# Kernel tuning notes

Measured on AMD Instinct MI355X. Metric: run time of the kernel, lower is better.

## Reference

```python
import jax, jax.numpy as jnp
import numpy as np

HIDDEN = 4096
N_HEADS = 16
HEAD_DIM = HIDDEN // N_HEADS  # 256
ROTARY_DIM = 64
ROPE_THETA = 10000.0


def _rope_cos_sin(positions):
    # positions: [S] int -> cos/sin: [S, ROTARY_DIM//2]
    inv_freq = 1.0 / (ROPE_THETA ** (jnp.arange(0, ROTARY_DIM, 2, dtype=jnp.float32) / ROTARY_DIM))
    angles = positions.astype(jnp.float32)[:, None] * inv_freq[None, :]
    return jnp.cos(angles), jnp.sin(angles)


def _apply_rope_interleaved(x, cos, sin):
    # x: [B, S, H, D]; rotate first ROTARY_DIM dims, GPT-J (non-neox) interleaved pairs
    xr = x[..., :ROTARY_DIM]
    x1 = xr[..., 0::2]
    x2 = xr[..., 1::2]
    c = cos[None, :, None, :]
    s = sin[None, :, None, :]
    o1 = x1 * c - x2 * s
    o2 = x1 * s + x2 * c
    rot = jnp.stack([o1, o2], axis=-1).reshape(xr.shape)
    return jnp.concatenate([rot, x[..., ROTARY_DIM:]], axis=-1)


def setup_inputs() -> dict:
    key = jax.random.key(0)
    k1, k2, k3 = jax.random.split(key, 3)
    B, S = 2, 2048
    hidden_states = jax.random.normal(k1, (B, S, HIDDEN), dtype=jnp.float32)
    positions = jnp.arange(S, dtype=jnp.int32)
    w_qkv = jax.random.normal(k2, (3 * HIDDEN, HIDDEN), dtype=jnp.float32) * 0.02
    w_out = jax.random.normal(k3, (HIDDEN, HIDDEN), dtype=jnp.float32) * 0.02
    return {"hidden_states": hidden_states, "positions": positions, "w_qkv": w_qkv, "w_out": w_out}


def reference(hidden_states, positions, w_qkv, w_out):
    B, S, H = hidden_states.shape
    qkv = jnp.einsum("bsh,oh->bso", hidden_states, w_qkv)  # [B,S,3H]
    q, k, v = jnp.split(qkv, 3, axis=-1)
    q = q.reshape(B, S, N_HEADS, HEAD_DIM)
    k = k.reshape(B, S, N_HEADS, HEAD_DIM)
    v = v.reshape(B, S, N_HEADS, HEAD_DIM)
    cos, sin = _rope_cos_sin(positions)
    q = _apply_rope_interleaved(q, cos, sin)
    k = _apply_rope_interleaved(k, cos, sin)
    scale = HEAD_DIM ** -0.5
    scores = jnp.einsum("bqhd,bkhd->bhqk", q, k) * scale  # [B,nh,S,S]
    causal = jnp.tril(jnp.ones((S, S), dtype=bool))
    scores = jnp.where(causal[None, None], scores, jnp.finfo(scores.dtype).min)
    probs = jax.nn.softmax(scores, axis=-1)
    attn = jnp.einsum("bhqk,bkhd->bqhd", probs, v).reshape(B, S, H)
    return jnp.einsum("bsh,oh->bso", attn, w_out)
```

## Files before the change

kernel.cpp:

```cpp
#include <hip/hip_runtime.h>

typedef __attribute__((ext_vector_type(8))) short short8;
typedef __attribute__((ext_vector_type(4))) float f32x4;

__device__ __forceinline__ unsigned short f2bf(float f) {
    union { float f; unsigned int u; } v; v.f = f;
    unsigned int u = v.u;
    unsigned int r = (u + 0x7FFFu + ((u >> 16) & 1u)) >> 16;
    return (unsigned short)r;
}
__device__ __forceinline__ float bf2f(unsigned short u) {
    union { unsigned int u; float f; } v; v.u = ((unsigned int)u) << 16;
    return v.f;
}
__device__ __forceinline__ void load_lds16(const void* g, void* l) {
    __builtin_amdgcn_global_load_lds(
        (const __attribute__((address_space(1))) void*)g,
        (__attribute__((address_space(3))) void*)l, 16, 0, 0);
}
#define FENCE() asm volatile("" ::: "memory")
#define BAR() do { FENCE(); __builtin_amdgcn_s_barrier(); FENCE(); } while (0)

__device__ __forceinline__ int swz(int o) { return o ^ ((o >> 3) & 0x70); }

__global__ __launch_bounds__(256) void conv_bf16(const float* __restrict__ in,
                                                 unsigned short* __restrict__ out, int n4) {
    int i = blockIdx.x * 256 + threadIdx.x;
    if (i >= n4) return;
    float4 v = ((const float4*)in)[i];
    ushort4 o;
    o.x = f2bf(v.x); o.y = f2bf(v.y); o.z = f2bf(v.z); o.w = f2bf(v.w);
    ((ushort4*)out)[i] = o;
}

template <bool OUT_BF16>
__global__ __launch_bounds__(512, 2) void gemm256(const unsigned short* __restrict__ A,
                                                  const unsigned short* __restrict__ B,
                                                  void* __restrict__ Cv,
                                                  int M, int N, int K, int NBN) {
    __shared__ __align__(16) char smem[131072];
    const int tid = threadIdx.x;
    const int lane = tid & 63, wv = tid >> 6;
    const int wm = wv >> 2, wn = wv & 3;
    const int fr = lane & 15, fo = (lane >> 4) * 8;

    const int nwg = gridDim.x, bid = blockIdx.x;
    const int q = nwg >> 3, r = nwg & 7, xcd = bid & 7, lid = bid >> 3;
    const int wg = (xcd < r ? xcd * (q + 1) : r * (q + 1) + (xcd - r) * q) + lid;
    const int bm = wg / NBN, bn = wg % NBN;

    const unsigned short* gA = A + (size_t)bm * 256 * K;
    const unsigned short* gB = B + (size_t)bn * 256 * K;

    int srow[2][2], scol[2][2];
#pragma unroll
    for (int h = 0; h < 2; ++h)
#pragma unroll
        for (int rr = 0; rr < 2; ++rr) {
            int o = h * 16384 + rr * 8192 + tid * 16;
            int osw = swz(o);
            srow[h][rr] = osw >> 7;
            scol[h][rr] = (osw & 127) >> 1;
        }

    f32x4 acc[8][4] = {};
    short8 a[4][2], b[4][2];

    auto STAGE = [&](const unsigned short* g, int regionBase, int h, int t) {
#pragma unroll
        for (int rr = 0; rr < 2; ++rr)
            load_lds16(g + (size_t)srow[h][rr] * K + t * 64 + scol[h][rr],
                       smem + regionBase + h * 16384 + rr * 8192 + tid * 16);
    };
    auto RDA = [&](int bufBase, int mh) {
#pragma unroll
        for (int mf = 0; mf < 4; ++mf)
#pragma unroll
            for (int ks = 0; ks < 2; ++ks) {
                int o = swz((wm * 128 + mh * 64 + mf * 16 + fr) * 128 + (ks * 32 + fo) * 2);
                a[mf][ks] = *(const short8*)(smem + bufBase + o);
            }
    };
    auto RDB = [&](int bufBase, int nh) {
#pragma unroll
        for (int jj = 0; jj < 2; ++jj)
#pragma unroll
            for (int ks = 0; ks < 2; ++ks) {
                int o = swz((wn * 64 + (nh * 2 + jj) * 16 + fr) * 128 + (ks * 32 + fo) * 2);
                b[nh * 2 + jj][ks] = *(const short8*)(smem + bufBase + 32768 + o);
            }
    };
    auto MM = [&](int mh, int nh) {
        __builtin_amdgcn_s_setprio(1);
#pragma unroll
        for (int mf = 0; mf < 4; ++mf)
#pragma unroll
            for (int jj = 0; jj < 2; ++jj)
#pragma unroll
                for (int ks = 0; ks < 2; ++ks)
                    acc[mh * 4 + mf][nh * 2 + jj] = __builtin_amdgcn_mfma_f32_16x16x32_bf16(
                        a[mf][ks], b[nh * 2 + jj][ks], acc[mh * 4 + mf][nh * 2 + jj], 0, 0, 0);
        __builtin_amdgcn_s_setprio(0);
    };

    const int A0 = 0, B0 = 32768, A1 = 65536, B1 = 98304;

    STAGE(gA, A0, 0, 0); STAGE(gA, A0, 1, 0);
    STAGE(gB, B0, 0, 0); STAGE(gB, B0, 1, 0);
    STAGE(gB, B1, 0, 1); STAGE(gB, B1, 1, 1);
    FENCE();
    asm volatile("s_waitcnt vmcnt(4)" ::: "memory");
    __builtin_amdgcn_s_barrier();
    FENCE();

    const int NIT = K >> 7;
    for (int i = 0; i < NIT; ++i) {
        const bool last = (i == NIT - 1);
        const int t0 = 2 * i, t1 = 2 * i + 1;
        RDA(A0, 0); RDB(A0, 0);
        STAGE(gA, A1, 0, t1);
        BAR(); MM(0, 0); BAR();
        RDB(A0, 1);
        STAGE(gA, A1, 1, t1);
        BAR(); MM(0, 1); BAR();
        RDA(A0, 1);
        if (!last) STAGE(gB, B0, 0, t0 + 2);
        BAR(); MM(1, 1); BAR();
        if (!last) STAGE(gB, B0, 1, t0 + 2);
        BAR(); MM(1, 0);
        FENCE();
        if (last) asm volatile("s_waitcnt vmcnt(0)" ::: "memory");
        else      asm volatile("s_waitcnt vmcnt(4)" ::: "memory");
        __builtin_amdgcn_s_barrier();
        FENCE();
        RDA(A1, 0); RDB(A1, 0);
        if (!last) STAGE(gA, A0, 0, t0 + 2);
        BAR(); MM(0, 0); BAR();
        RDB(A1, 1);
        if (!last) STAGE(gA, A0, 1, t0 + 2);
        BAR(); MM(0, 1); BAR();
        RDA(A1, 1);
        if (!last) STAGE(gB, B1, 0, t1 + 2);
        BAR(); MM(1, 1); BAR();
        if (!last) STAGE(gB, B1, 1, t1 + 2);
        BAR(); MM(1, 0);
        FENCE();
        if (!last) asm volatile("s_waitcnt vmcnt(4)" ::: "memory");
        __builtin_amdgcn_s_barrier();
        FENCE();
    }

    const size_t row0 = (size_t)bm * 256 + wm * 128 + ((lane >> 4) << 2);
    const int col0 = bn * 256 + wn * 64 + fr;
#pragma unroll
    for (int mf = 0; mf < 8; ++mf)
#pragma unroll
        for (int nf = 0; nf < 4; ++nf)
#pragma unroll
            for (int j = 0; j < 4; ++j) {
                size_t idx = (row0 + mf * 16 + j) * (size_t)N + col0 + nf * 16;
                if (OUT_BF16) ((unsigned short*)Cv)[idx] = f2bf(acc[mf][nf][j]);
                else          ((float*)Cv)[idx] = acc[mf][nf][j];
            }
}

__global__ __launch_bounds__(256) void rope_repack(const unsigned short* __restrict__ qkv,
                                                   const int* __restrict__ positions,
                                                   unsigned short* __restrict__ qp,
                                                   unsigned short* __restrict__ kp) {
    int r = blockIdx.x * 4 + (threadIdx.x >> 6);
    int h = r & 15, s = (r >> 4) & 2047, b = r >> 15;
    int d = (threadIdx.x & 63) * 4;
    const unsigned short* src = qkv + (size_t)(b * 2048 + s) * 12288 + h * 256 + d;
    ushort4 q = *(const ushort4*)src;
    ushort4 k = *(const ushort4*)(src + 4096);
    if (d < 64) {
        float pos = (float)positions[s];
        const float LF = 0.4152410118609203f;
        float i0 = (float)(d >> 1);
        float a0 = pos * exp2f(-i0 * LF);
        float a1 = pos * exp2f(-(i0 + 1.0f) * LF);
        float c0 = cosf(a0), s0 = sinf(a0), c1 = cosf(a1), s1 = sinf(a1);
        float qx = bf2f(q.x), qy = bf2f(q.y), qz = bf2f(q.z), qw = bf2f(q.w);
        q.x = f2bf(qx * c0 - qy * s0); q.y = f2bf(qx * s0 + qy * c0);
        q.z = f2bf(qz * c1 - qw * s1); q.w = f2bf(qz * s1 + qw * c1);
        float kx = bf2f(k.x), ky = bf2f(k.y), kz = bf2f(k.z), kw = bf2f(k.w);
        k.x = f2bf(kx * c0 - ky * s0); k.y = f2bf(kx * s0 + ky * c0);
        k.z = f2bf(kz * c1 - kw * s1); k.w = f2bf(kz * s1 + kw * c1);
    }
    size_t dst = ((size_t)((b * 16 + h) * 2048 + s)) * 256 + d;
    *(ushort4*)&qp[dst] = q;
    *(ushort4*)&kp[dst] = k;
}

__global__ __launch_bounds__(256) void v_transpose(const unsigned short* __restrict__ qkv,
                                                   unsigned short* __restrict__ vt) {
    int bid = blockIdx.x;
    int dt = bid & 3, st = (bid >> 2) & 31, bh = bid >> 7;
    int b = bh >> 4, h = bh & 15;
    __shared__ unsigned short t[64][72];
    int tid = threadIdx.x;
#pragma unroll
    for (int rep = 0; rep < 16; ++rep) {
        int idx = rep * 256 + tid;
        int r = idx >> 6, c = idx & 63;
        t[r][c] = qkv[(size_t)(b * 2048 + st * 64 + r) * 12288 + 8192 + h * 256 + dt * 64 + c];
    }
    __syncthreads();
#pragma unroll
    for (int rep = 0; rep < 16; ++rep) {
        int idx = rep * 256 + tid;
        int r = idx >> 6, c = idx & 63;
        vt[(size_t)(bh * 256 + dt * 64 + r) * 2048 + st * 64 + c] = t[c][r];
    }
}

__global__ __launch_bounds__(256) void attn_fwd(const unsigned short* __restrict__ Qp,
                                                const unsigned short* __restrict__ Kp,
                                                const unsigned short* __restrict__ Vt,
                                                unsigned short* __restrict__ Oa) {
    __shared__ __align__(16) unsigned short Ks[32 * 256];
    __shared__ __align__(16) unsigned short Vs[256 * 32];
    __shared__ __align__(16) unsigned short Ps[4][16 * 32];
    const int tid = threadIdx.x, lane = tid & 63, wv = tid >> 6;
    const int bh = blockIdx.x, qt = blockIdx.y;
    const int fr = lane & 15, fo = (lane >> 4) * 8;
    const unsigned short* Qb = Qp + (size_t)bh * 2048 * 256;
    const unsigned short* Kb = Kp + (size_t)bh * 2048 * 256;
    const unsigned short* Vb = Vt + (size_t)bh * 256 * 2048;
    const int qbase = qt * 64 + wv * 16;

    short8 qf[8];
#pragma unroll
    for (int c = 0; c < 8; ++c)
        qf[c] = *(const short8*)&Qb[(size_t)(qbase + fr) * 256 + c * 32 + fo];

    f32x4 o_acc[16] = {};
    float m_run[4] = {-1e30f, -1e30f, -1e30f, -1e30f};
    float l_run[4] = {0.f, 0.f, 0.f, 0.f};

    const int nkv = qt * 64 + 64;
    for (int kv0 = 0; kv0 < nkv; kv0 += 32) {
#pragma unroll
        for (int i = 0; i < 4; ++i) {
            int eb = (wv * 4 + i) * 512;
            load_lds16(&Kb[(size_t)(kv0 + (eb >> 8) + (lane >> 5)) * 256 + (lane & 31) * 8], &Ks[eb]);
        }
#pragma unroll
        for (int i = 0; i < 4; ++i) {
            int eb = (wv * 4 + i) * 512;
            load_lds16(&Vb[(size_t)((eb >> 5) + (lane >> 2)) * 2048 + kv0 + (lane & 3) * 8], &Vs[eb]);
        }
        __syncthreads();

        f32x4 sc[2] = {};
#pragma unroll
        for (int t = 0; t < 2; ++t)
#pragma unroll
            for (int c = 0; c < 8; ++c) {
                short8 kf = *(const short8*)&Ks[(t * 16 + fr) * 256 + c * 32 + fo];
                sc[t] = __builtin_amdgcn_mfma_f32_16x16x32_bf16(qf[c], kf, sc[t], 0, 0, 0);
            }

        float sv[2][4];
#pragma unroll
        for (int j = 0; j < 4; ++j) {
            int qi = qbase + ((lane >> 4) << 2) + j;
#pragma unroll
            for (int t = 0; t < 2; ++t) {
                float x = sc[t][j] * 0.0625f;
                int kvi = kv0 + t * 16 + fr;
                sv[t][j] = (kvi > qi) ? -1e30f : x;
            }
            float pm = fmaxf(sv[0][j], sv[1][j]);
#pragma unroll
            for (int off = 1; off < 16; off <<= 1)
                pm = fmaxf(pm, __shfl_xor(pm, off));
            float mn = fmaxf(m_run[j], pm);
            float al = __expf(m_run[j] - mn);
            m_run[j] = mn;
            float rs = 0.f;
#pragma unroll
            for (int t = 0; t < 2; ++t) {
                float p = __expf(sv[t][j] - mn);
                rs += p;
                Ps[wv][(((lane >> 4) << 2) + j) * 32 + t * 16 + fr] = f2bf(p);
            }
#pragma unroll
            for (int off = 1; off < 16; off <<= 1)
                rs += __shfl_xor(rs, off);
            l_run[j] = l_run[j] * al + rs;
#pragma unroll
            for (int n = 0; n < 16; ++n) o_acc[n][j] *= al;
        }

        short8 pf = *(const short8*)&Ps[wv][fr * 32 + fo];
#pragma unroll
        for (int n = 0; n < 16; ++n) {
            short8 vf = *(const short8*)&Vs[(n * 16 + fr) * 32 + fo];
            o_acc[n] = __builtin_amdgcn_mfma_f32_16x16x32_bf16(pf, vf, o_acc[n], 0, 0, 0);
        }
        __syncthreads();
    }

    const int b = bh >> 4, h = bh & 15;
#pragma unroll
    for (int j = 0; j < 4; ++j) {
        float inv = 1.0f / l_run[j];
        int qrow = qbase + ((lane >> 4) << 2) + j;
        size_t base = ((size_t)(b * 2048 + qrow)) * 4096 + h * 256;
#pragma unroll
        for (int n = 0; n < 16; ++n)
            Oa[base + n * 16 + fr] = f2bf(o_acc[n][j] * inv);
    }
}

extern "C" void kernel_launch(void* const* d_in, const int* in_sizes, int n_in,
                              void* d_out, int out_size, void* d_ws, size_t ws_size,
                              hipStream_t stream) {
    const float* hidden = (const float*)d_in[0];
    const int* positions = (const int*)d_in[1];
    const float* w_qkv = (const float*)d_in[2];
    const float* w_out = (const float*)d_in[3];
    float* out = (float*)d_out;

    const size_t MB32 = 33554432;
    char* ws = (char*)d_ws;
    unsigned short* hidden_bf = (unsigned short*)ws;
    unsigned short* wqkv_bf   = (unsigned short*)(ws + MB32);
    unsigned short* qkv_bf    = (unsigned short*)(ws + 4 * MB32);
    unsigned short* qp  = wqkv_bf;
    unsigned short* kp  = wqkv_bf + 16777216;
    unsigned short* vtp = wqkv_bf + 33554432;
    unsigned short* attn_bf = hidden_bf;
    unsigned short* wout_bf = qkv_bf;

    conv_bf16<<<16384, 256, 0, stream>>>(hidden, hidden_bf, 4194304);
    conv_bf16<<<49152, 256, 0, stream>>>(w_qkv, wqkv_bf, 12582912);

    gemm256<true><<<16 * 48, 512, 0, stream>>>(hidden_bf, wqkv_bf, qkv_bf, 4096, 12288, 4096, 48);

    rope_repack<<<16384, 256, 0, stream>>>(qkv_bf, positions, qp, kp);
    v_transpose<<<4096, 256, 0, stream>>>(qkv_bf, vtp);

    attn_fwd<<<dim3(32, 32), 256, 0, stream>>>(qp, kp, vtp, attn_bf);

    conv_bf16<<<16384, 256, 0, stream>>>(w_out, wout_bf, 4194304);
    gemm256<false><<<16 * 16, 512, 0, stream>>>(attn_bf, wout_bf, out, 4096, 4096, 4096, 16);
}
```

Before: 853.1 us.

## Restructure GEMM main loop pipeline with fewer barriers and deeper prefetch

Reschedules the 256x256 bf16 GEMM main loop. The A1 tile is now prefetched in the prologue, and LDS fragment reads for the next step are issued before the MFMA block of the current step. The number of barriers per iteration is roughly halved, and vmcnt waits move to fewer points. The aim is to cut barrier stalls and to overlap LDS reads and global-to-LDS staging with the matrix math. The cost is tighter buffer-reuse ordering, which risks LDS read/write hazards if a wait count is wrong.

```diff
diff --git a/kernel.cpp b/kernel.cpp
--- a/kernel.cpp
+++ b/kernel.cpp
@@ -18,8 +18,8 @@
         (const __attribute__((address_space(1))) void*)g,
         (__attribute__((address_space(3))) void*)l, 16, 0, 0);
 }
-#define FENCE() asm volatile("" ::: "memory")
-#define BAR() do { FENCE(); __builtin_amdgcn_s_barrier(); FENCE(); } while (0)
+#define BAR() asm volatile("s_barrier" ::: "memory")
+#define WAITV(n) asm volatile("s_waitcnt vmcnt(" #n ")" ::: "memory")
 
 __device__ __forceinline__ int swz(int o) { return o ^ ((o >> 3) & 0x70); }
 
@@ -108,46 +108,54 @@
     STAGE(gA, A0, 0, 0); STAGE(gA, A0, 1, 0);
     STAGE(gB, B0, 0, 0); STAGE(gB, B0, 1, 0);
     STAGE(gB, B1, 0, 1); STAGE(gB, B1, 1, 1);
-    FENCE();
-    asm volatile("s_waitcnt vmcnt(4)" ::: "memory");
-    __builtin_amdgcn_s_barrier();
-    FENCE();
+    STAGE(gA, A1, 0, 1); STAGE(gA, A1, 1, 1);
+    WAITV(8);
+    BAR();
+    RDA(A0, 0);
+    RDB(A0, 0);
 
     const int NIT = K >> 7;
     for (int i = 0; i < NIT; ++i) {
         const bool last = (i == NIT - 1);
-        const int t0 = 2 * i, t1 = 2 * i + 1;
-        RDA(A0, 0); RDB(A0, 0);
-        STAGE(gA, A1, 0, t1);
-        BAR(); MM(0, 0); BAR();
+        const int t2 = 2 * i + 2, t3 = 2 * i + 3;
         RDB(A0, 1);
-        STAGE(gA, A1, 1, t1);
-        BAR(); MM(0, 1); BAR();
+        MM(0, 0);
+        if (i > 0) STAGE(gA, A1, 1, 2 * i + 1);
+        BAR();
+        MM(0, 1);
         RDA(A0, 1);
-        if (!last) STAGE(gB, B0, 0, t0 + 2);
-        BAR(); MM(1, 1); BAR();
-        if (!last) STAGE(gB, B0, 1, t0 + 2);
-        BAR(); MM(1, 0);
-        FENCE();
-        if (last) asm volatile("s_waitcnt vmcnt(0)" ::: "memory");
-        else      asm volatile("s_waitcnt vmcnt(4)" ::: "memory");
-        __builtin_amdgcn_s_barrier();
-        FENCE();
+        BAR();
+        MM(1, 1);
+        if (!last) {
+            STAGE(gB, B0, 0, t2);
+            WAITV(2);
+        } else {
+            WAITV(0);
+        }
+        BAR();
+        MM(1, 0);
         RDA(A1, 0); RDB(A1, 0);
-        if (!last) STAGE(gA, A0, 0, t0 + 2);
-        BAR(); MM(0, 0); BAR();
+        if (!last) { STAGE(gB, B0, 1, t2); STAGE(gA, A0, 0, t2); }
+        BAR();
         RDB(A1, 1);
-        if (!last) STAGE(gA, A0, 1, t0 + 2);
-        BAR(); MM(0, 1); BAR();
+        MM(0, 0);
+        if (!last) STAGE(gA, A0, 1, t2);
+        BAR();
+        MM(0, 1);
         RDA(A1, 1);
-        if (!last) STAGE(gB, B1, 0, t1 + 2);
-        BAR(); MM(1, 1); BAR();
-        if (!last) STAGE(gB, B1, 1, t1 + 2);
-        BAR(); MM(1, 0);
-        FENCE();
-        if (!last) asm volatile("s_waitcnt vmcnt(4)" ::: "memory");
-        __builtin_amdgcn_s_barrier();
-        FENCE();
+        BAR();
+        MM(1, 1);
+        if (!last) {
+            STAGE(gB, B1, 0, t3);
+            WAITV(2);
+        }
+        BAR();
+        MM(1, 0);
+        if (!last) {
+            RDA(A0, 0); RDB(A0, 0);
+            STAGE(gB, B1, 1, t3); STAGE(gA, A1, 0, t3);
+        }
+        BAR();
     }
 
     const size_t row0 = (size_t)bm * 256 + wm * 128 + ((lane >> 4) << 2);
```

After: 867.2 us. Within noise of the previous version (+1.7%).
